# Optimization experiments

Measured on AMD Instinct MI355X. Metric: run time of the kernel, lower is better.

## Reference

```python
import jax, jax.numpy as jnp
import numpy as np

BSZ, SEQ, HID = 4, 2048, 2048
NH, NKV, HD = 16, 8, 128
SLOTS, MAXSEQ = 8, 4096
EPS = 1e-6
SCALE = HD ** -0.5


def rms_norm(x, w):
    # normalize over last dim (head_dim)
    var = jnp.mean(jnp.square(x), axis=-1, keepdims=True)
    return x * jax.lax.rsqrt(var + EPS) * w


def setup_inputs() -> dict:
    key = jax.random.key(0)
    ks = jax.random.split(key, 6)
    return {
        "hidden_states": jax.random.normal(ks[0], (BSZ, SEQ, HID), jnp.float32),
        "positions": jnp.tile(jnp.arange(SEQ, dtype=jnp.int32)[None, :], (BSZ, 1)),
        "k_cache": jnp.zeros((SLOTS, MAXSEQ, NKV, HD), jnp.float32),
        "v_cache": jnp.zeros((SLOTS, MAXSEQ, NKV, HD), jnp.float32),
        "slot_mapping": jnp.arange(BSZ, dtype=jnp.int32),
        "kv_start_indices": jnp.zeros((BSZ,), jnp.int32),
        "seq_lens": jnp.full((BSZ,), SEQ, jnp.int32),
        "qkv_w": jax.random.normal(ks[1], ((NH + 2 * NKV) * HD, HID), jnp.float32) * 0.02,
        "qkv_b": jax.random.normal(ks[2], ((NH + 2 * NKV) * HD,), jnp.float32) * 0.02,
        "o_w": jax.random.normal(ks[3], (HID, NH * HD), jnp.float32) * 0.02,
        "q_norm_w": jnp.ones((HD,), jnp.float32),
        "k_norm_w": jnp.ones((HD,), jnp.float32),
    }


def reference(hidden_states, positions, k_cache, v_cache, slot_mapping,
              kv_start_indices, seq_lens, qkv_w, qkv_b, o_w, q_norm_w, k_norm_w):
    bsz, seq_len, _ = hidden_states.shape
    qkv = jnp.einsum("bsh,oh->bso", hidden_states, qkv_w) + qkv_b
    q, k, v = jnp.split(qkv, [NH * HD, NH * HD + NKV * HD], axis=-1)
    q = rms_norm(q.reshape(bsz, seq_len, NH, HD), q_norm_w)
    k = rms_norm(k.reshape(bsz, seq_len, NKV, HD), k_norm_w)
    v = v.reshape(bsz, seq_len, NKV, HD)

    # paged KV cache scatter: cache[slot, start:start+seq] = k/v  (vectorized over batch)
    rows = kv_start_indices[:, None] + jnp.arange(seq_len)[None, :]  # [B,S]
    k_cache = k_cache.at[slot_mapping[:, None], rows].set(k)
    v_cache = v_cache.at[slot_mapping[:, None], rows].set(v)

    # prefill path (seq_len > 1): gather back up to max_l (= seq_len here, static)
    max_l = seq_len
    k_h = k_cache[slot_mapping, :max_l].transpose(0, 2, 1, 3)  # [B,Hkv,L,D]
    v_h = v_cache[slot_mapping, :max_l].transpose(0, 2, 1, 3)
    n_rep = NH // NKV
    if n_rep > 1:  # repeat_interleave over head dim (GQA)
        k_h = jnp.repeat(k_h, n_rep, axis=1)
        v_h = jnp.repeat(v_h, n_rep, axis=1)

    qh = q.transpose(0, 2, 1, 3)  # [B,H,S,D]
    scores = jnp.einsum("bhqd,bhkd->bhqk", qh, k_h) * SCALE
    causal = jnp.tril(jnp.ones((seq_len, max_l), bool))
    scores = jnp.where(causal[None, None], scores, -jnp.inf)
    attn = jax.nn.softmax(scores, axis=-1)
    out = jnp.einsum("bhqk,bhkd->bhqd", attn, v_h)
    out = out.transpose(0, 2, 1, 3).reshape(bsz, seq_len, NH * HD)
    return jnp.einsum("bso,ho->bsh", out, o_w)
```

## Files before the change

### kernel.cpp

```cpp
#include <hip/hip_runtime.h>
#include <hip/hip_bf16.h>
#include <stdint.h>

typedef unsigned short u16;
typedef __attribute__((ext_vector_type(8))) __bf16 bf16x8;
typedef __attribute__((ext_vector_type(4))) float f32x4;

#define EPSF 1e-6f
#define SCALE 0.08838834764831845f

__device__ __forceinline__ u16 f2bf(float f) {
    union { float f; uint32_t u; } a; a.f = f;
    uint32_t r = a.u + 0x7FFFu + ((a.u >> 16) & 1u);
    return (u16)(r >> 16);
}
__device__ __forceinline__ float bf2f(u16 u) {
    union { uint32_t u; float f; } a; a.u = ((uint32_t)u) << 16;
    return a.f;
}
__device__ __forceinline__ u16 f2bf_n(float f) {
    __hip_bfloat16 h = __float2bfloat16(f);
    return *reinterpret_cast<u16*>(&h);
}

__global__ __launch_bounds__(256) void cvt_f32_bf16_k(
    const float* __restrict__ in, u16* __restrict__ out, long n4)
{
    long i = (long)blockIdx.x * 256 + threadIdx.x;
    if (i >= n4) return;
    float4 v = ((const float4*)in)[i];
    ushort4 o;
    o.x = f2bf(v.x); o.y = f2bf(v.y); o.z = f2bf(v.z); o.w = f2bf(v.w);
    ((ushort4*)out)[i] = o;
}

__device__ __forceinline__ void gload16(const u16* g, u16* l) {
    __builtin_amdgcn_global_load_lds(
        (const __attribute__((address_space(1))) uint32_t*)g,
        (__attribute__((address_space(3))) uint32_t*)l, 16, 0, 0);
}

__global__ __launch_bounds__(512, 2) void gemm8_nt(
    const u16* __restrict__ A, const u16* __restrict__ B,
    const float* __restrict__ bias,
    float* __restrict__ Cf, u16* __restrict__ Cb,
    int M, int N, int K)
{
    __shared__ u16 As[2][256 * 64];
    __shared__ u16 Bs[2][256 * 64];

    const int t = threadIdx.x;
    const int lane = t & 63;
    const int g = lane >> 4, lr = lane & 15;
    const int w = t >> 6;
    const int wm = w >> 2, wn = w & 3;

    const int nwg = gridDim.x * gridDim.y;
    const int bid0 = blockIdx.y * gridDim.x + blockIdx.x;
    const int cpx = nwg >> 3;
    const int bids = (bid0 & 7) * cpx + (bid0 >> 3);
    const int bn = (bids % gridDim.x) * 256;
    const int bm = (bids / gridDim.x) * 256;
    const int NT = K >> 6;

    f32x4 z = {0.f, 0.f, 0.f, 0.f};
    f32x4 acc[8][4];
#pragma unroll
    for (int m = 0; m < 8; ++m)
#pragma unroll
        for (int n = 0; n < 4; ++n) acc[m][n] = z;

    auto STAGE2 = [&](int buf, int k0, int p) {
#pragma unroll
        for (int j = 0; j < 2; ++j) {
            int idx = p * 1024 + j * 512 + t;
            int ci = idx & 2047;
            int row = ci >> 3, slot = ci & 7;
            int csrc = slot ^ (row & 7);
            if (idx < 2048)
                gload16(A + (size_t)(bm + row) * K + k0 + csrc * 8, &As[buf][0] + ci * 8);
            else
                gload16(B + (size_t)(bn + row) * K + k0 + csrc * 8, &Bs[buf][0] + ci * 8);
        }
    };

    bf16x8 afr0[4][2], afr1[4][2];
    bf16x8 bf0[2][2], bf1[2][2];

#pragma unroll
    for (int p = 0; p < 4; ++p) STAGE2(0, 0, p);

    for (int kt = 0; kt < NT; ++kt) {
        const int cur = kt & 1;
        const int k0n = (kt + 1) << 6;
        const bool last = (kt == NT - 1);
        const char* Ab = (const char*)&As[cur][0];
        const char* Bb = (const char*)&Bs[cur][0];
        const int swz = (lr & 7) << 4;

        auto LDA = [&](bf16x8 (&dst)[4][2], int mbase) {
#pragma unroll
            for (int mi = 0; mi < 4; ++mi) {
                int row = wm * 128 + (mbase + mi) * 16 + lr;
#pragma unroll
                for (int kc = 0; kc < 2; ++kc)
                    dst[mi][kc] = *(const bf16x8*)(Ab + row * 128 + ((kc * 64 + g * 16) ^ swz));
            }
        };
        auto LDB = [&](bf16x8 (&dst)[2][2], int nbase) {
#pragma unroll
            for (int ni = 0; ni < 2; ++ni) {
                int row = wn * 64 + (nbase + ni) * 16 + lr;
#pragma unroll
                for (int kc = 0; kc < 2; ++kc)
                    dst[ni][kc] = *(const bf16x8*)(Bb + row * 128 + ((kc * 64 + g * 16) ^ swz));
            }
        };
        auto MMA = [&](bf16x8 (&amf)[4][2], int mf0, int nf0, bf16x8 (&bfr)[2][2]) {
            __builtin_amdgcn_s_setprio(1);
#pragma unroll
            for (int mi = 0; mi < 4; ++mi)
#pragma unroll
                for (int ni = 0; ni < 2; ++ni)
#pragma unroll
                    for (int kc = 0; kc < 2; ++kc)
                        acc[mf0 + mi][nf0 + ni] = __builtin_amdgcn_mfma_f32_16x16x32_bf16(
                            amf[mi][kc], bfr[ni][kc], acc[mf0 + mi][nf0 + ni], 0, 0, 0);
            __builtin_amdgcn_s_setprio(0);
        };

        if (!last) {
#pragma unroll
            for (int p = 0; p < 4; ++p) STAGE2(cur ^ 1, k0n, p);
            asm volatile("s_waitcnt vmcnt(8)" ::: "memory");
        } else {
            asm volatile("s_waitcnt vmcnt(0)" ::: "memory");
        }
        __builtin_amdgcn_s_barrier();
        __builtin_amdgcn_sched_barrier(0);

        LDA(afr0, 0); LDB(bf0, 0); LDB(bf1, 2);
        MMA(afr0, 0, 0, bf0);
        MMA(afr0, 0, 2, bf1);
        LDA(afr1, 4);
        MMA(afr1, 4, 2, bf1);
        MMA(afr1, 4, 0, bf0);

        __builtin_amdgcn_sched_barrier(0);
        __builtin_amdgcn_s_barrier();
    }

#pragma unroll
    for (int mf = 0; mf < 8; ++mf) {
#pragma unroll
        for (int nf = 0; nf < 4; ++nf) {
            int col = bn + wn * 64 + nf * 16 + lr;
            float bv = bias ? bias[col] : 0.f;
#pragma unroll
            for (int r = 0; r < 4; ++r) {
                int row = bm + wm * 128 + mf * 16 + g * 4 + r;
                float v = acc[mf][nf][r] + bv;
                if (Cf) Cf[(size_t)row * N + col] = v;
                else    Cb[(size_t)row * N + col] = f2bf(v);
            }
        }
    }
}

__global__ __launch_bounds__(256) void rmsnorm_k(
    u16* __restrict__ qkv, const float* __restrict__ qw, const float* __restrict__ kw)
{
    const int row = blockIdx.x;
    const int w = threadIdx.x >> 6, l = threadIdx.x & 63;
#pragma unroll
    for (int i = 0; i < 6; ++i) {
        int head = w + i * 4;
        const float* wt = (head < 16) ? qw : kw;
        u16* p = qkv + (size_t)row * 4096 + head * 128;
        uint32_t u = *(const uint32_t*)(p + l * 2);
        float x0 = bf2f((u16)(u & 0xFFFF));
        float x1 = bf2f((u16)(u >> 16));
        float ss = x0 * x0 + x1 * x1;
#pragma unroll
        for (int m = 1; m < 64; m <<= 1) ss += __shfl_xor(ss, m, 64);
        float inv = rsqrtf(ss * (1.0f / 128.0f) + EPSF);
        float r0 = x0 * inv * wt[l * 2];
        float r1 = x1 * inv * wt[l * 2 + 1];
        uint32_t o = (uint32_t)f2bf(r0) | ((uint32_t)f2bf(r1) << 16);
        *(uint32_t*)(p + l * 2) = o;
    }
}

__global__ __launch_bounds__(256) void vtrans_k(
    const u16* __restrict__ qkv, u16* __restrict__ vt)
{
    __shared__ u16 T[64 * 64];
    const int t = threadIdx.x;
    const int sx = blockIdx.x * 64;
    const int dy = blockIdx.y * 64;
    const int z  = blockIdx.z;
    const int b = z >> 3, hk = z & 7;
#pragma unroll
    for (int j = 0; j < 2; ++j) {
        int idx = t + j * 256;
        int r = idx >> 3, c8 = (idx & 7) * 8;
        uint4 v = *(const uint4*)(qkv + (size_t)(b * 2048 + sx + r) * 4096 + 3072 + hk * 128 + dy + c8);
        int slot = (c8 >> 3) ^ ((r ^ (r >> 3)) & 7);
        *(uint4*)(&T[r * 64 + slot * 8]) = v;
    }
    __syncthreads();
#pragma unroll
    for (int j = 0; j < 2; ++j) {
        int idx = t + j * 256;
        int rr = idx >> 3, cc8 = (idx & 7) * 8;
        u16 tmp[8];
#pragma unroll
        for (int i = 0; i < 8; ++i) {
            int row = cc8 + i;
            int slot = (rr >> 3) ^ ((row ^ (row >> 3)) & 7);
            tmp[i] = T[row * 64 + slot * 8 + (rr & 7)];
        }
        *(uint4*)(vt + ((size_t)z * 128 + dy + rr) * 2048 + sx + cc8) = *(uint4*)tmp;
    }
}

#define P_S 72

__global__ __launch_bounds__(256, 2) void attn5_k(
    const u16* __restrict__ qkv, const u16* __restrict__ vt,
    u16* __restrict__ aout)
{
    __shared__ u16 Kt[2][64 * 128];
    __shared__ u16 Vl[2][128 * 64];
    __shared__ u16 P[4][16 * P_S];

    const int t = threadIdx.x;
    const int lane = t & 63;
    const int w = t >> 6;
    const int g = lane >> 4, lr = lane & 15;
    const int pr = blockIdx.x, h = blockIdx.y, b = blockIdx.z;
    const int hk = h >> 1;
    const size_t rowb = (size_t)b * 2048;

    const u16* ksrc = qkv + rowb * 4096 + 2048 + hk * 128;
    const u16* vsrc = vt + (size_t)(b * 8 + hk) * 128 * 2048;

    bf16x8 ones8;
    {
        union { bf16x8 v; u16 e[8]; } on;
#pragma unroll
        for (int j = 0; j < 8; ++j) on.e[j] = 0x3F80;
        ones8 = on.v;
    }

    auto STAGE = [&](int buf, int kvb) {
#pragma unroll
        for (int j = 0; j < 4; ++j) {
            int idx = t + j * 256;
            {
                int row = idx >> 4, slot = idx & 15;
                int csrc = (slot & 8) | ((slot & 7) ^ (row & 7));
                gload16(ksrc + (size_t)(kvb + row) * 4096 + csrc * 8, &Kt[buf][0] + idx * 8);
            }
            {
                int row = idx >> 3, slot = idx & 7;
                int csrc = slot ^ (row & 7);
                gload16(vsrc + (size_t)row * 2048 + kvb + csrc * 8, &Vl[buf][0] + idx * 8);
            }
        }
    };

    for (int sub = 0; sub < 2; ++sub) {
        const int qt = sub ? 15 - pr : pr;
        const int qbase = qt * 128;
        const int nt = 2 * qt + 2;

        bf16x8 qf[2][4];
        {
            const u16* qp = qkv + (rowb + qbase + w * 32 + lr) * 4096 + h * 128;
#pragma unroll
            for (int sb = 0; sb < 2; ++sb)
#pragma unroll
                for (int c = 0; c < 4; ++c) {
                    union { bf16x8 v; u16 e[8]; } uq;
                    uq.v = *(const bf16x8*)(qp + sb * 16 * 4096 + c * 32 + g * 8);
#pragma unroll
                    for (int jj = 0; jj < 8; ++jj) uq.e[jj] = f2bf(bf2f(uq.e[jj]) * SCALE);
                    qf[sb][c] = uq.v;
                }
        }

        float m_r[2][4];
        f32x4 z = {0.f, 0.f, 0.f, 0.f};
        f32x4 l_acc[2];
        f32x4 o_acc[2][8];
#pragma unroll
        for (int sb = 0; sb < 2; ++sb) {
#pragma unroll
            for (int r = 0; r < 4; ++r) m_r[sb][r] = -INFINITY;
            l_acc[sb] = z;
#pragma unroll
            for (int d = 0; d < 8; ++d) o_acc[sb][d] = z;
        }

        STAGE(0, 0);

        for (int kt = 0; kt < nt; ++kt) {
            const int cur = kt & 1;
            const int kvb = kt * 64;
            if (kt + 1 < nt) {
                STAGE(cur ^ 1, kvb + 64);
                asm volatile("s_waitcnt vmcnt(8)" ::: "memory");
            } else {
                asm volatile("s_waitcnt vmcnt(0)" ::: "memory");
            }
            __builtin_amdgcn_s_barrier();
            __builtin_amdgcn_sched_barrier(0);

            const u16* Kc = &Kt[cur][0];
            const u16* Vc = &Vl[cur][0];
            const bool active = !(kt == nt - 1 && w < 2);
            const bool near = (kt >= nt - 2);

            if (active) {
                f32x4 s[2][4];
                __builtin_amdgcn_s_setprio(1);
#pragma unroll
                for (int cb = 0; cb < 4; ++cb) {
                    int row = cb * 16 + lr;
                    s[0][cb] = z; s[1][cb] = z;
#pragma unroll
                    for (int c = 0; c < 4; ++c) {
                        int chunk = c * 4 + g;
                        int slot = (chunk & 8) | ((chunk & 7) ^ (row & 7));
                        bf16x8 kf = *(const bf16x8*)(&Kc[row * 128 + slot * 8]);
                        s[0][cb] = __builtin_amdgcn_mfma_f32_16x16x32_bf16(qf[0][c], kf, s[0][cb], 0, 0, 0);
                        s[1][cb] = __builtin_amdgcn_mfma_f32_16x16x32_bf16(qf[1][c], kf, s[1][cb], 0, 0, 0);
                    }
                }
                __builtin_amdgcn_s_setprio(0);

#pragma unroll
                for (int sb = 0; sb < 2; ++sb) {
#pragma unroll
                    for (int r = 0; r < 4; ++r) {
                        float v0 = s[sb][0][r], v1 = s[sb][1][r], v2 = s[sb][2][r], v3 = s[sb][3][r];
                        if (near) {
                            int qa = qbase + w * 32 + sb * 16 + g * 4 + r;
                            if (kvb + lr > qa)      v0 = -INFINITY;
                            if (kvb + 16 + lr > qa) v1 = -INFINITY;
                            if (kvb + 32 + lr > qa) v2 = -INFINITY;
                            if (kvb + 48 + lr > qa) v3 = -INFINITY;
                        }
                        float mx = fmaxf(fmaxf(v0, v1), fmaxf(v2, v3));
                        mx = fmaxf(mx, __shfl_xor(mx, 1));
                        mx = fmaxf(mx, __shfl_xor(mx, 2));
                        mx = fmaxf(mx, __shfl_xor(mx, 4));
                        mx = fmaxf(mx, __shfl_xor(mx, 8));
                        float mold = m_r[sb][r];
                        float mbase;
                        if (__all(mx <= mold + 8.0f)) {
                            mbase = mold;
                        } else {
                            float mnew = fmaxf(mold, mx);
                            float alpha = __expf(mold - mnew);
                            l_acc[sb][r] *= alpha;
#pragma unroll
                            for (int d = 0; d < 8; ++d) o_acc[sb][d][r] *= alpha;
                            m_r[sb][r] = mnew;
                            mbase = mnew;
                        }
                        float p0 = __expf(v0 - mbase), p1 = __expf(v1 - mbase);
                        float p2 = __expf(v2 - mbase), p3 = __expf(v3 - mbase);
                        int prow = (g * 4 + r) * P_S;
                        P[w][prow + lr]      = f2bf_n(p0);
                        P[w][prow + 16 + lr] = f2bf_n(p1);
                        P[w][prow + 32 + lr] = f2bf_n(p2);
                        P[w][prow + 48 + lr] = f2bf_n(p3);
                    }

#pragma unroll
                    for (int kk = 0; kk < 2; ++kk) {
                        bf16x8 pa = *(const bf16x8*)(&P[w][lr * P_S + kk * 32 + g * 8]);
                        __builtin_amdgcn_s_setprio(1);
                        l_acc[sb] = __builtin_amdgcn_mfma_f32_16x16x32_bf16(pa, ones8, l_acc[sb], 0, 0, 0);
#pragma unroll
                        for (int d = 0; d < 8; ++d) {
                            int row = d * 16 + lr;
                            int slot = (kk * 4 + g) ^ (row & 7);
                            bf16x8 vf = *(const bf16x8*)(&Vc[row * 64 + slot * 8]);
                            o_acc[sb][d] = __builtin_amdgcn_mfma_f32_16x16x32_bf16(pa, vf, o_acc[sb][d], 0, 0, 0);
                        }
                        __builtin_amdgcn_s_setprio(0);
                    }
                }
            }

            __builtin_amdgcn_sched_barrier(0);
            __builtin_amdgcn_s_barrier();
        }

#pragma unroll
        for (int sb = 0; sb < 2; ++sb) {
            const int qrow0 = qbase + w * 32 + sb * 16 + g * 4;
#pragma unroll
            for (int r = 0; r < 4; ++r) {
                float inv = 1.0f / l_acc[sb][r];
                u16* op = aout + (rowb + qrow0 + r) * 2048 + h * 128;
#pragma unroll
                for (int d = 0; d < 8; ++d)
                    op[d * 16 + lr] = f2bf_n(o_acc[sb][d][r] * inv);
            }
        }
    }
}

extern "C" void kernel_launch(void* const* d_in, const int* in_sizes, int n_in,
                              void* d_out, int out_size, void* d_ws, size_t ws_size,
                              hipStream_t stream)
{
    const float* hidden = (const float*)d_in[0];
    const float* qkv_w = (const float*)d_in[7];
    const float* qkv_b = (const float*)d_in[8];
    const float* o_w   = (const float*)d_in[9];
    const float* q_nw  = (const float*)d_in[10];
    const float* k_nw  = (const float*)d_in[11];

    char* ws = (char*)d_ws;
    u16* hid_bf  = (u16*)ws; ws += (size_t)8192 * 2048 * 2;
    u16* wqkv_bf = (u16*)ws; ws += (size_t)4096 * 2048 * 2;
    u16* ow_bf   = (u16*)ws; ws += (size_t)2048 * 2048 * 2;
    u16* qkv_bf  = (u16*)ws; ws += (size_t)8192 * 4096 * 2;
    u16* attn_bf = (u16*)ws; ws += (size_t)8192 * 2048 * 2;
    u16* vt_bf   = hid_bf;

    cvt_f32_bf16_k<<<16384, 256, 0, stream>>>(hidden, hid_bf, 4194304L);
    cvt_f32_bf16_k<<<8192, 256, 0, stream>>>(qkv_w, wqkv_bf, 2097152L);
    cvt_f32_bf16_k<<<4096, 256, 0, stream>>>(o_w, ow_bf, 1048576L);

    gemm8_nt<<<dim3(16, 32), 512, 0, stream>>>(hid_bf, wqkv_bf, qkv_b,
                                               nullptr, qkv_bf, 8192, 4096, 2048);
    rmsnorm_k<<<dim3(8192), 256, 0, stream>>>(qkv_bf, q_nw, k_nw);
    vtrans_k<<<dim3(32, 2, 32), 256, 0, stream>>>(qkv_bf, vt_bf);
    attn5_k<<<dim3(8, 16, 4), 256, 0, stream>>>(qkv_bf, vt_bf, attn_bf);
    gemm8_nt<<<dim3(8, 32), 512, 0, stream>>>(attn_bf, ow_bf, nullptr,
                                              (float*)d_out, nullptr, 8192, 2048, 2048);
}
```

Before: 415.9 us.

## Single-buffer attention tiles and launch one block per query tile

The attention kernel drops double-buffered K/V shared memory and the prefetch of the next tile, loading each tile synchronously before computing on it. Launch bounds rise to three blocks per CU. The paired short/long query-tile work per block is replaced by one block per query tile, longest tiles first, doubling the grid. This aims for higher occupancy and more blocks to balance load, but gives up in-block overlap of global loads with MFMA compute and lowers the register budget per thread.

```diff
diff --git a/kernel.cpp b/kernel.cpp
--- a/kernel.cpp
+++ b/kernel.cpp
@@ -226,19 +226,20 @@
 
 #define P_S 72
 
-__global__ __launch_bounds__(256, 2) void attn5_k(
+__global__ __launch_bounds__(256, 3) void attn6_k(
     const u16* __restrict__ qkv, const u16* __restrict__ vt,
     u16* __restrict__ aout)
 {
-    __shared__ u16 Kt[2][64 * 128];
-    __shared__ u16 Vl[2][128 * 64];
+    __shared__ u16 Kt[64 * 128];
+    __shared__ u16 Vl[128 * 64];
     __shared__ u16 P[4][16 * P_S];
 
     const int t = threadIdx.x;
     const int lane = t & 63;
     const int w = t >> 6;
     const int g = lane >> 4, lr = lane & 15;
-    const int pr = blockIdx.x, h = blockIdx.y, b = blockIdx.z;
+    const int h = blockIdx.y, b = blockIdx.z;
+    const int qt = 15 - blockIdx.x;
     const int hk = h >> 1;
     const size_t rowb = (size_t)b * 2048;
 
@@ -253,164 +254,151 @@
         ones8 = on.v;
     }
 
-    auto STAGE = [&](int buf, int kvb) {
+    auto STAGE = [&](int kvb) {
 #pragma unroll
         for (int j = 0; j < 4; ++j) {
             int idx = t + j * 256;
             {
                 int row = idx >> 4, slot = idx & 15;
                 int csrc = (slot & 8) | ((slot & 7) ^ (row & 7));
-                gload16(ksrc + (size_t)(kvb + row) * 4096 + csrc * 8, &Kt[buf][0] + idx * 8);
+                gload16(ksrc + (size_t)(kvb + row) * 4096 + csrc * 8, &Kt[0] + idx * 8);
             }
             {
                 int row = idx >> 3, slot = idx & 7;
                 int csrc = slot ^ (row & 7);
-                gload16(vsrc + (size_t)row * 2048 + kvb + csrc * 8, &Vl[buf][0] + idx * 8);
+                gload16(vsrc + (size_t)row * 2048 + kvb + csrc * 8, &Vl[0] + idx * 8);
             }
         }
     };
 
-    for (int sub = 0; sub < 2; ++sub) {
-        const int qt = sub ? 15 - pr : pr;
-        const int qbase = qt * 128;
-        const int nt = 2 * qt + 2;
-
-        bf16x8 qf[2][4];
-        {
-            const u16* qp = qkv + (rowb + qbase + w * 32 + lr) * 4096 + h * 128;
-#pragma unroll
-            for (int sb = 0; sb < 2; ++sb)
+    const int qbase = qt * 128;
+    const int nt = 2 * qt + 2;
+
+    bf16x8 qf[2][4];
+    {
+        const u16* qp = qkv + (rowb + qbase + w * 32 + lr) * 4096 + h * 128;
+#pragma unroll
+        for (int sb = 0; sb < 2; ++sb)
+#pragma unroll
+            for (int c = 0; c < 4; ++c) {
+                union { bf16x8 v; u16 e[8]; } uq;
+                uq.v = *(const bf16x8*)(qp + sb * 16 * 4096 + c * 32 + g * 8);
+#pragma unroll
+                for (int jj = 0; jj < 8; ++jj) uq.e[jj] = f2bf(bf2f(uq.e[jj]) * SCALE);
+                qf[sb][c] = uq.v;
+            }
+    }
+
+    float m_r[2][4];
+    f32x4 z = {0.f, 0.f, 0.f, 0.f};
+    f32x4 l_acc[2];
+    f32x4 o_acc[2][8];
+#pragma unroll
+    for (int sb = 0; sb < 2; ++sb) {
+#pragma unroll
+        for (int r = 0; r < 4; ++r) m_r[sb][r] = -INFINITY;
+        l_acc[sb] = z;
+#pragma unroll
+        for (int d = 0; d < 8; ++d) o_acc[sb][d] = z;
+    }
+
+    for (int kt = 0; kt < nt; ++kt) {
+        const int kvb = kt * 64;
+        __syncthreads();
+        STAGE(kvb);
+        asm volatile("s_waitcnt vmcnt(0)" ::: "memory");
+        __builtin_amdgcn_s_barrier();
+        __builtin_amdgcn_sched_barrier(0);
+
+        const bool active = !(kt == nt - 1 && w < 2);
+        const bool near = (kt >= nt - 2);
+
+        if (active) {
+            f32x4 s[2][4];
+            __builtin_amdgcn_s_setprio(1);
+#pragma unroll
+            for (int cb = 0; cb < 4; ++cb) {
+                int row = cb * 16 + lr;
+                s[0][cb] = z; s[1][cb] = z;
 #pragma unroll
                 for (int c = 0; c < 4; ++c) {
-                    union { bf16x8 v; u16 e[8]; } uq;
-                    uq.v = *(const bf16x8*)(qp + sb * 16 * 4096 + c * 32 + g * 8);
-#pragma unroll
-                    for (int jj = 0; jj < 8; ++jj) uq.e[jj] = f2bf(bf2f(uq.e[jj]) * SCALE);
-                    qf[sb][c] = uq.v;
+                    int chunk = c * 4 + g;
+                    int slot = (chunk & 8) | ((chunk & 7) ^ (row & 7));
+                    bf16x8 kf = *(const bf16x8*)(&Kt[row * 128 + slot * 8]);
+                    s[0][cb] = __builtin_amdgcn_mfma_f32_16x16x32_bf16(qf[0][c], kf, s[0][cb], 0, 0, 0);
+                    s[1][cb] = __builtin_amdgcn_mfma_f32_16x16x32_bf16(qf[1][c], kf, s[1][cb], 0, 0, 0);
                 }
-        }
-
-        float m_r[2][4];
-        f32x4 z = {0.f, 0.f, 0.f, 0.f};
-        f32x4 l_acc[2];
-        f32x4 o_acc[2][8];
-#pragma unroll
-        for (int sb = 0; sb < 2; ++sb) {
-#pragma unroll
-            for (int r = 0; r < 4; ++r) m_r[sb][r] = -INFINITY;
-            l_acc[sb] = z;
-#pragma unroll
-            for (int d = 0; d < 8; ++d) o_acc[sb][d] = z;
-        }
-
-        STAGE(0, 0);
-
-        for (int kt = 0; kt < nt; ++kt) {
-            const int cur = kt & 1;
-            const int kvb = kt * 64;
-            if (kt + 1 < nt) {
-                STAGE(cur ^ 1, kvb + 64);
-                asm volatile("s_waitcnt vmcnt(8)" ::: "memory");
-            } else {
-                asm volatile("s_waitcnt vmcnt(0)" ::: "memory");
-            }
-            __builtin_amdgcn_s_barrier();
-            __builtin_amdgcn_sched_barrier(0);
-
-            const u16* Kc = &Kt[cur][0];
-            const u16* Vc = &Vl[cur][0];
-            const bool active = !(kt == nt - 1 && w < 2);
-            const bool near = (kt >= nt - 2);
-
-            if (active) {
-                f32x4 s[2][4];
-                __builtin_amdgcn_s_setprio(1);
-#pragma unroll
-                for (int cb = 0; cb < 4; ++cb) {
-                    int row = cb * 16 + lr;
-                    s[0][cb] = z; s[1][cb] = z;
-#pragma unroll
-                    for (int c = 0; c < 4; ++c) {
-                        int chunk = c * 4 + g;
-                        int slot = (chunk & 8) | ((chunk & 7) ^ (row & 7));
-                        bf16x8 kf = *(const bf16x8*)(&Kc[row * 128 + slot * 8]);
-                        s[0][cb] = __builtin_amdgcn_mfma_f32_16x16x32_bf16(qf[0][c], kf, s[0][cb], 0, 0, 0);
-                        s[1][cb] = __builtin_amdgcn_mfma_f32_16x16x32_bf16(qf[1][c], kf, s[1][cb], 0, 0, 0);
+            }
+            __builtin_amdgcn_s_setprio(0);
+
+#pragma unroll
+            for (int sb = 0; sb < 2; ++sb) {
+#pragma unroll
+                for (int r = 0; r < 4; ++r) {
+                    float v0 = s[sb][0][r], v1 = s[sb][1][r], v2 = s[sb][2][r], v3 = s[sb][3][r];
+                    if (near) {
+                        int qa = qbase + w * 32 + sb * 16 + g * 4 + r;
+                        if (kvb + lr > qa)      v0 = -INFINITY;
+                        if (kvb + 16 + lr > qa) v1 = -INFINITY;
+                        if (kvb + 32 + lr > qa) v2 = -INFINITY;
+                        if (kvb + 48 + lr > qa) v3 = -INFINITY;
                     }
+                    float mx = fmaxf(fmaxf(v0, v1), fmaxf(v2, v3));
+                    mx = fmaxf(mx, __shfl_xor(mx, 1));
+                    mx = fmaxf(mx, __shfl_xor(mx, 2));
+                    mx = fmaxf(mx, __shfl_xor(mx, 4));
+                    mx = fmaxf(mx, __shfl_xor(mx, 8));
+                    float mold = m_r[sb][r];
+                    float mbase;
+                    if (__all(mx <= mold + 8.0f)) {
+                        mbase = mold;
+                    } else {
+                        float mnew = fmaxf(mold, mx);
+                        float alpha = __expf(mold - mnew);
+                        l_acc[sb][r] *= alpha;
+#pragma unroll
+                        for (int d = 0; d < 8; ++d) o_acc[sb][d][r] *= alpha;
+                        m_r[sb][r] = mnew;
+                        mbase = mnew;
+                    }
+                    float p0 = __expf(v0 - mbase), p1 = __expf(v1 - mbase);
+                    float p2 = __expf(v2 - mbase), p3 = __expf(v3 - mbase);
+                    int prow = (g * 4 + r) * P_S;
+                    P[w][prow + lr]      = f2bf_n(p0);
+                    P[w][prow + 16 + lr] = f2bf_n(p1);
+                    P[w][prow + 32 + lr] = f2bf_n(p2);
+                    P[w][prow + 48 + lr] = f2bf_n(p3);
                 }
-                __builtin_amdgcn_s_setprio(0);
-
-#pragma unroll
-                for (int sb = 0; sb < 2; ++sb) {
-#pragma unroll
-                    for (int r = 0; r < 4; ++r) {
-                        float v0 = s[sb][0][r], v1 = s[sb][1][r], v2 = s[sb][2][r], v3 = s[sb][3][r];
-                        if (near) {
-                            int qa = qbase + w * 32 + sb * 16 + g * 4 + r;
-                            if (kvb + lr > qa)      v0 = -INFINITY;
-                            if (kvb + 16 + lr > qa) v1 = -INFINITY;
-                            if (kvb + 32 + lr > qa) v2 = -INFINITY;
-                            if (kvb + 48 + lr > qa) v3 = -INFINITY;
-                        }
-                        float mx = fmaxf(fmaxf(v0, v1), fmaxf(v2, v3));
-                        mx = fmaxf(mx, __shfl_xor(mx, 1));
-                        mx = fmaxf(mx, __shfl_xor(mx, 2));
-                        mx = fmaxf(mx, __shfl_xor(mx, 4));
-                        mx = fmaxf(mx, __shfl_xor(mx, 8));
-                        float mold = m_r[sb][r];
-                        float mbase;
-                        if (__all(mx <= mold + 8.0f)) {
-                            mbase = mold;
-                        } else {
-                            float mnew = fmaxf(mold, mx);
-                            float alpha = __expf(mold - mnew);
-                            l_acc[sb][r] *= alpha;
-#pragma unroll
-                            for (int d = 0; d < 8; ++d) o_acc[sb][d][r] *= alpha;
-                            m_r[sb][r] = mnew;
-                            mbase = mnew;
-                        }
-                        float p0 = __expf(v0 - mbase), p1 = __expf(v1 - mbase);
-                        float p2 = __expf(v2 - mbase), p3 = __expf(v3 - mbase);
-                        int prow = (g * 4 + r) * P_S;
-                        P[w][prow + lr]      = f2bf_n(p0);
-                        P[w][prow + 16 + lr] = f2bf_n(p1);
-                        P[w][prow + 32 + lr] = f2bf_n(p2);
-                        P[w][prow + 48 + lr] = f2bf_n(p3);
+
+#pragma unroll
+                for (int kk = 0; kk < 2; ++kk) {
+                    bf16x8 pa = *(const bf16x8*)(&P[w][lr * P_S + kk * 32 + g * 8]);
+                    __builtin_amdgcn_s_setprio(1);
+                    l_acc[sb] = __builtin_amdgcn_mfma_f32_16x16x32_bf16(pa, ones8, l_acc[sb], 0, 0, 0);
+#pragma unroll
+                    for (int d = 0; d < 8; ++d) {
+                        int row = d * 16 + lr;
+                        int slot = (kk * 4 + g) ^ (row & 7);
+                        bf16x8 vf = *(const bf16x8*)(&Vl[row * 64 + slot * 8]);
+                        o_acc[sb][d] = __builtin_amdgcn_mfma_f32_16x16x32_bf16(pa, vf, o_acc[sb][d], 0, 0, 0);
                     }
-
-#pragma unroll
-                    for (int kk = 0; kk < 2; ++kk) {
-                        bf16x8 pa = *(const bf16x8*)(&P[w][lr * P_S + kk * 32 + g * 8]);
-                        __builtin_amdgcn_s_setprio(1);
-                        l_acc[sb] = __builtin_amdgcn_mfma_f32_16x16x32_bf16(pa, ones8, l_acc[sb], 0, 0, 0);
-#pragma unroll
-                        for (int d = 0; d < 8; ++d) {
-                            int row = d * 16 + lr;
-                            int slot = (kk * 4 + g) ^ (row & 7);
-                            bf16x8 vf = *(const bf16x8*)(&Vc[row * 64 + slot * 8]);
-                            o_acc[sb][d] = __builtin_amdgcn_mfma_f32_16x16x32_bf16(pa, vf, o_acc[sb][d], 0, 0, 0);
-                        }
-                        __builtin_amdgcn_s_setprio(0);
-                    }
+                    __builtin_amdgcn_s_setprio(0);
                 }
             }
-
-            __builtin_amdgcn_sched_barrier(0);
-            __builtin_amdgcn_s_barrier();
-        }
-
-#pragma unroll
-        for (int sb = 0; sb < 2; ++sb) {
-            const int qrow0 = qbase + w * 32 + sb * 16 + g * 4;
-#pragma unroll
-            for (int r = 0; r < 4; ++r) {
-                float inv = 1.0f / l_acc[sb][r];
-                u16* op = aout + (rowb + qrow0 + r) * 2048 + h * 128;
-#pragma unroll
-                for (int d = 0; d < 8; ++d)
-                    op[d * 16 + lr] = f2bf_n(o_acc[sb][d][r] * inv);
-            }
+        }
+        __builtin_amdgcn_sched_barrier(0);
+    }
+
+#pragma unroll
+    for (int sb = 0; sb < 2; ++sb) {
+        const int qrow0 = qbase + w * 32 + sb * 16 + g * 4;
+#pragma unroll
+        for (int r = 0; r < 4; ++r) {
+            float inv = 1.0f / l_acc[sb][r];
+            u16* op = aout + (rowb + qrow0 + r) * 2048 + h * 128;
+#pragma unroll
+            for (int d = 0; d < 8; ++d)
+                op[d * 16 + lr] = f2bf_n(o_acc[sb][d][r] * inv);
         }
     }
 }
@@ -442,7 +430,7 @@
                                                nullptr, qkv_bf, 8192, 4096, 2048);
     rmsnorm_k<<<dim3(8192), 256, 0, stream>>>(qkv_bf, q_nw, k_nw);
     vtrans_k<<<dim3(32, 2, 32), 256, 0, stream>>>(qkv_bf, vt_bf);
-    attn5_k<<<dim3(8, 16, 4), 256, 0, stream>>>(qkv_bf, vt_bf, attn_bf);
+    attn6_k<<<dim3(16, 16, 4), 256, 0, stream>>>(qkv_bf, vt_bf, attn_bf);
     gemm8_nt<<<dim3(8, 32), 512, 0, stream>>>(attn_bf, ow_bf, nullptr,
                                               (float*)d_out, nullptr, 8192, 2048, 2048);
 }
```

Result: slower. 621.7 us (+49.5%).
